# Performance work log

Measured on AMD Instinct MI355X. Metric: run time of the kernel, lower is better.

## Reference

```python
import jax, jax.numpy as jnp
import numpy as np

N = 100000      # nodes
EG = 600000     # global (knn) edges used by GAT layers
E = 600000      # prediction edges scored by edge_mlp
H = 1           # gat_heads
C = 64          # hidden_dim (per-head out channels)
HC = H * C
EDGE_IN = 2 * HC + 2  # 130
EDGE_HID = EDGE_IN * 4  # 520


def gat_layer(x, W, att_src, att_dst, bias, src, dst):
    # PyG GATConv (concat=True, residual=False, no edge_dim, eval mode)
    n = x.shape[0]
    h = (x @ W).reshape(n, H, C)                      # [N,H,C]
    a_s = jnp.sum(h * att_src, axis=-1)               # [N,H]
    a_d = jnp.sum(h * att_dst, axis=-1)               # [N,H]
    alpha = jax.nn.leaky_relu(a_s[src] + a_d[dst], 0.2)  # [Eg,H]
    amax = jax.ops.segment_max(alpha, dst, num_segments=n)
    amax = jnp.where(jnp.isfinite(amax), amax, 0.0)
    e = jnp.exp(alpha - amax[dst])
    denom = jax.ops.segment_sum(e, dst, num_segments=n)
    w = e / (denom[dst] + 1e-16)                      # scatter-softmax over in-edges of dst
    out = jax.ops.segment_sum(h[src] * w[:, :, None], dst, num_segments=n)
    return out.reshape(n, HC) + bias


def setup_inputs() -> dict:
    key = jax.random.key(0)
    ks = jax.random.split(key, 16)
    glorot = lambda k, shape: jax.random.normal(k, shape, jnp.float32) * np.sqrt(2.0 / (shape[0] + shape[-1]))
    inp = {
        "pos": jax.random.normal(ks[0], (N, 3), jnp.float32),
        "edge_index": jax.random.randint(ks[1], (2, E), 0, N, jnp.int32),
        "global_edge_index": jax.random.randint(ks[2], (2, EG), 0, N, jnp.int32),
        "edge_attr": jax.random.uniform(ks[3], (E, 2), jnp.float32),
        # GAT layer 0 (in=3)
        "W0": glorot(ks[4], (3, HC)),
        "att_src0": glorot(ks[5], (1, H, C)),
        "att_dst0": glorot(ks[6], (1, H, C)),
        "b0": jnp.zeros((HC,), jnp.float32),
        # GAT layer 1 (in=HC)
        "W1": glorot(ks[7], (HC, HC)),
        "att_src1": glorot(ks[8], (1, H, C)),
        "att_dst1": glorot(ks[9], (1, H, C)),
        "b1": jnp.zeros((HC,), jnp.float32),
        # edge MLP: Linear(130,520) -> ELU -> Linear(520,1)
        "Wm1": glorot(ks[10], (EDGE_IN, EDGE_HID)),
        "bm1": jnp.zeros((EDGE_HID,), jnp.float32),
        "Wm2": glorot(ks[11], (EDGE_HID, 1)),
        "bm2": jnp.zeros((1,), jnp.float32),
    }
    return inp


def reference(pos, edge_index, global_edge_index, edge_attr,
              W0, att_src0, att_dst0, b0,
              W1, att_src1, att_dst1, b1,
              Wm1, bm1, Wm2, bm2):
    gsrc, gdst = global_edge_index[0], global_edge_index[1]
    x = pos  # dropout p=0 -> identity
    x = jax.nn.elu(gat_layer(x, W0, att_src0, att_dst0, b0, gsrc, gdst))
    x = jax.nn.elu(gat_layer(x, W1, att_src1, att_dst1, b1, gsrc, gdst))
    # per-edge gather-concat-MLP
    esrc, edst = edge_index[0], edge_index[1]
    ef = jnp.concatenate([x[esrc], x[edst], edge_attr], axis=1)  # [E, 130]
    h = jax.nn.elu(ef @ Wm1 + bm1)
    edge_values = (h @ Wm2 + bm2)[:, 0]  # [E]
    return edge_values
```

## Files before the change

kernel.cpp:

```cpp
#include <hip/hip_runtime.h>

#define KN 100000
#define KEG 600000
#define KE 600000
#define NB 98
#define LOG2E 1.4426950408889634f
#define LN2 0.6931471805599453f

#define FB_PREP 391
#define FB_CVEC 33
#define FB_HIST 2344
#define FB_T0 25000

using u16 = unsigned short;
typedef __bf16 bf16x8 __attribute__((ext_vector_type(8)));
typedef float f32x4 __attribute__((ext_vector_type(4)));
typedef float f32x2 __attribute__((ext_vector_type(2)));

__device__ __forceinline__ float b2f(u16 u) { return __uint_as_float(((unsigned)u) << 16); }
__device__ __forceinline__ u16 f2b(float f) {
  unsigned u = __float_as_uint(f);
  u += 0x7FFF + ((u >> 16) & 1);
  return (u16)(u >> 16);
}
__device__ __forceinline__ int imin(int a, int b) { return a < b ? a : b; }
__device__ __forceinline__ float fexp2(float x) {
#if __has_builtin(__builtin_amdgcn_exp2f)
  return __builtin_amdgcn_exp2f(x);
#else
  return __expf(x * LN2);
#endif
}

__device__ __forceinline__ void gload_lds16(const void* g, void* l) {
  __builtin_amdgcn_global_load_lds(
      (const __attribute__((address_space(1))) unsigned int*)g,
      (__attribute__((address_space(3))) unsigned int*)l,
      16, 0, 0);
}

__global__ __launch_bounds__(256) void k_front(
    const float* __restrict__ pos, const float* __restrict__ W0,
    const float* __restrict__ att_s, const float* __restrict__ att_d,
    const float* __restrict__ wm1, const float* __restrict__ bm1,
    const float* __restrict__ wm2, const float* __restrict__ w1,
    const int* __restrict__ gdst,
    u16* __restrict__ wm1t, u16* __restrict__ w1t, float2* __restrict__ wsc2,
    float* __restrict__ w2sum, int* __restrict__ counts,
    u16* __restrict__ h, float* __restrict__ a_s, float* __restrict__ a_d) {
  int bid = blockIdx.x;
  if (bid < FB_PREP) {
    int idx = bid * 256 + threadIdx.x;
    if (idx < 33 * 5 * 512) {
      int j = idx & 7;
      int lane = (idx >> 3) & 63;
      int f = (idx >> 9) % 5;
      int nt = idx / (512 * 5);
      int n = nt * 16 + (lane & 15);
      float v = 0.f;
      if (n < 520) {
        if (f < 4) {
          int k = f * 32 + (lane >> 4) * 8 + j;
          v = wm1[k * 520 + n] * LOG2E;
        } else {
          int kk = (lane >> 4) * 8 + j;
          if (kk == 0) v = wm1[128 * 520 + n] * LOG2E;
          else if (kk == 1) v = wm1[129 * 520 + n] * LOG2E;
          else if (kk == 2) v = bm1[n] * LOG2E;
        }
      }
      wm1t[idx] = f2b(v);
    }
    if (idx < 33 * 64) {
      int lane = idx & 63, nt = idx >> 6;
      int col = nt * 16 + (lane & 15);
      float w2 = (col < 520) ? wm2[col] : 0.f;
      float2 p; p.x = w2; p.y = -LN2 * w2;
      wsc2[idx] = p;
    }
    if (idx < 4 * 2 * 64 * 8) {
      int j = idx & 7;
      int lane = (idx >> 3) & 63;
      int kt = (idx >> 9) & 1;
      int nt = idx >> 10;
      int n = nt * 16 + (lane & 15);
      int k = kt * 32 + (lane >> 4) * 8 + j;
      w1t[idx] = f2b(w1[k * 64 + n]);
    }
  } else if (bid < FB_PREP + FB_CVEC) {
    int lane = threadIdx.x & 63;
    int w = (bid - FB_PREP) * 4 + (threadIdx.x >> 6);
    float x = 0.f;
    if (w <= 129) {
      const float* row = wm1 + (size_t)w * 520;
#pragma unroll
      for (int j = 0; j < 8; ++j) x += row[j * 64 + lane] * wm2[j * 64 + lane];
      if (lane < 8) x += row[512 + lane] * wm2[512 + lane];
    } else if (w == 130) {
#pragma unroll
      for (int j = 0; j < 8; ++j) x += bm1[j * 64 + lane] * wm2[j * 64 + lane];
      if (lane < 8) x += bm1[512 + lane] * wm2[512 + lane];
    } else if (w == 131) {
#pragma unroll
      for (int j = 0; j < 8; ++j) x += wm2[j * 64 + lane];
      if (lane < 8) x += wm2[512 + lane];
    }
    for (int off = 1; off < 64; off <<= 1) x += __shfl_xor(x, off);
    if (w <= 130 && lane < 16) {
      int f = w >> 5, kk = w & 31;
      int qq = kk >> 3, jj = kk & 7;
      u16 chi = f2b(x);
      float v = (lane == 0) ? x : (lane == 1 ? (x - b2f(chi)) : 0.f);
      wm1t[(33 * 5 + f) * 512 + (qq * 16 + lane) * 8 + jj] = f2b(v);
    } else if (w == 131 && lane == 0) {
      w2sum[0] = x;
    }
  } else if (bid < FB_PREP + FB_CVEC + FB_HIST) {
    int e = (bid - (FB_PREP + FB_CVEC)) * 256 + threadIdx.x;
    if (e < KEG) atomicAdd(counts + gdst[e], 1);
  } else {
    int lane = threadIdx.x & 63;
    int n = (bid - (FB_PREP + FB_CVEC + FB_HIST)) * 4 + (threadIdx.x >> 6);
    float p0 = pos[n * 3 + 0], p1 = pos[n * 3 + 1], p2 = pos[n * 3 + 2];
    float hv = p0 * W0[lane] + p1 * W0[64 + lane] + p2 * W0[128 + lane];
    h[n * 64 + lane] = f2b(hv);
    float s = hv * att_s[lane];
    float d = hv * att_d[lane];
    for (int off = 1; off < 64; off <<= 1) { s += __shfl_xor(s, off); d += __shfl_xor(d, off); }
    if (lane == 0) { a_s[n] = s; a_d[n] = d; }
  }
}


__global__ __launch_bounds__(1024) void k_scan_block(
    const int* __restrict__ counts, int* __restrict__ incl, int* __restrict__ bsum) {
  int gid = blockIdx.x * 1024 + threadIdx.x;
  int lane = threadIdx.x & 63, w = threadIdx.x >> 6;
  int x = (gid < KN) ? counts[gid] : 0;
  for (int off = 1; off < 64; off <<= 1) {
    int y = __shfl_up(x, off);
    if (lane >= off) x += y;
  }
  __shared__ int wtot[16];
  if (lane == 63) wtot[w] = x;
  __syncthreads();
  if (w == 0 && lane < 16) {
    int t = wtot[lane];
    for (int off = 1; off < 16; off <<= 1) {
      int y = __shfl_up(t, off);
      if (lane >= off) t += y;
    }
    wtot[lane] = t;
  }
  __syncthreads();
  if (w > 0) x += wtot[w - 1];
  if (gid < KN) incl[gid] = x;
  if (threadIdx.x == 1023) bsum[blockIdx.x] = x;
}

__global__ __launch_bounds__(64) void k_scan_bsum(const int* __restrict__ bsum, int* __restrict__ boff) {
  int lane = threadIdx.x;
  int x0 = (lane < NB) ? bsum[lane] : 0;
  int x1 = (64 + lane < NB) ? bsum[64 + lane] : 0;
  int i0 = x0, i1 = x1;
  for (int off = 1; off < 64; off <<= 1) {
    int y0 = __shfl_up(i0, off), y1 = __shfl_up(i1, off);
    if (lane >= off) { i0 += y0; i1 += y1; }
  }
  int tot0 = __shfl(i0, 63);
  if (lane < NB) boff[lane] = i0 - x0;
  if (64 + lane < NB) boff[64 + lane] = i1 - x1 + tot0;
}

__global__ __launch_bounds__(1024) void k_scan_final(
    const int* __restrict__ incl, const int* __restrict__ counts,
    const int* __restrict__ boff, int* __restrict__ row_start) {
  int gid = blockIdx.x * 1024 + threadIdx.x;
  if (gid < KN) row_start[gid] = incl[gid] - counts[gid] + boff[blockIdx.x];
}

__global__ __launch_bounds__(256) void k_fill(
    const int* __restrict__ gsrc, const int* __restrict__ gdst,
    const int* __restrict__ row_start, int* __restrict__ cursor,
    int* __restrict__ csr_src) {
  int e = blockIdx.x * 256 + threadIdx.x;
  if (e >= KEG) return;
  int d = gdst[e];
  int pos = atomicAdd(cursor + d, 1);
  csr_src[row_start[d] + pos] = gsrc[e];
}


__global__ __launch_bounds__(256) void k_transform1(
    const u16* __restrict__ x, const u16* __restrict__ w1t,
    const float* __restrict__ att_s, const float* __restrict__ att_d,
    u16* __restrict__ h, float* __restrict__ a_s, float* __restrict__ a_d) {
  int lane = threadIdx.x & 63;
  int wave = threadIdx.x >> 6;
  int nodebase = blockIdx.x * 64 + wave * 16;
  int m = lane & 15, q = lane >> 4;

  int node = imin(nodebase + m, KN - 1);
  const bf16x8* px = (const bf16x8*)(x + node * 64);
  bf16x8 A0 = px[q];
  bf16x8 A1 = px[q + 4];

  const bf16x8* bt = (const bf16x8*)w1t;
  float ps[4] = {0.f, 0.f, 0.f, 0.f};
  float pd[4] = {0.f, 0.f, 0.f, 0.f};
#pragma unroll
  for (int nt = 0; nt < 4; ++nt) {
    int col = nt * 16 + m;
    float asv = att_s[col], adv = att_d[col];
    f32x4 acc = {0.f, 0.f, 0.f, 0.f};
    acc = __builtin_amdgcn_mfma_f32_16x16x32_bf16(A0, bt[(nt * 2 + 0) * 64 + lane], acc, 0, 0, 0);
    acc = __builtin_amdgcn_mfma_f32_16x16x32_bf16(A1, bt[(nt * 2 + 1) * 64 + lane], acc, 0, 0, 0);
#pragma unroll
    for (int r = 0; r < 4; ++r) {
      int rown = nodebase + q * 4 + r;
      if (rown < KN) h[rown * 64 + col] = f2b(acc[r]);
      ps[r] += acc[r] * asv;
      pd[r] += acc[r] * adv;
    }
  }
#pragma unroll
  for (int r = 0; r < 4; ++r) {
    float s = ps[r], d = pd[r];
    s += __shfl_xor(s, 1); d += __shfl_xor(d, 1);
    s += __shfl_xor(s, 2); d += __shfl_xor(d, 2);
    s += __shfl_xor(s, 4); d += __shfl_xor(d, 4);
    s += __shfl_xor(s, 8); d += __shfl_xor(d, 8);
    int rown = nodebase + q * 4 + r;
    if (m == 0 && rown < KN) { a_s[rown] = s; a_d[rown] = d; }
  }
}

__global__ __launch_bounds__(256) void k_gat_agg(
    const int* __restrict__ row_start, const int* __restrict__ counts,
    const int* __restrict__ csr_src, const float* __restrict__ a_s,
    const float* __restrict__ a_d, const u16* __restrict__ h,
    const float* __restrict__ bias, u16* __restrict__ xout) {
  int lane = threadIdx.x & 63;
  int n = blockIdx.x * 4 + (threadIdx.x >> 6);
  int start = row_start[n], deg = counts[n];
  float adn = a_d[n];
  float acc = 0.f, den = 0.f;
  int j = 0;
  for (; j + 4 <= deg; j += 4) {
    int s0 = csr_src[start + j];
    int s1 = csr_src[start + j + 1];
    int s2 = csr_src[start + j + 2];
    int s3 = csr_src[start + j + 3];
    float al0 = a_s[s0] + adn; al0 = al0 > 0.f ? al0 : 0.2f * al0;
    float al1 = a_s[s1] + adn; al1 = al1 > 0.f ? al1 : 0.2f * al1;
    float al2 = a_s[s2] + adn; al2 = al2 > 0.f ? al2 : 0.2f * al2;
    float al3 = a_s[s3] + adn; al3 = al3 > 0.f ? al3 : 0.2f * al3;
    float w0 = __expf(al0), w1 = __expf(al1);
    float w2 = __expf(al2), w3 = __expf(al3);
    float h0 = b2f(h[s0 * 64 + lane]);
    float h1 = b2f(h[s1 * 64 + lane]);
    float h2 = b2f(h[s2 * 64 + lane]);
    float h3 = b2f(h[s3 * 64 + lane]);
    den += (w0 + w1) + (w2 + w3);
    acc += w0 * h0 + w1 * h1 + w2 * h2 + w3 * h3;
  }
  for (; j < deg; ++j) {
    int s0 = csr_src[start + j];
    float al = a_s[s0] + adn; al = al > 0.f ? al : 0.2f * al;
    float w0 = __expf(al);
    den += w0;
    acc += w0 * b2f(h[s0 * 64 + lane]);
  }
  float v = acc / (den + 1e-16f) + bias[lane];
  v = v > 0.f ? v : expm1f(v);
  xout[n * 64 + lane] = f2b(v);
}

__global__ __launch_bounds__(256) void k_edge_mlp(
    const int* __restrict__ eidx, const u16* __restrict__ x2bf,
    const float* __restrict__ eattr, const u16* __restrict__ wm1t,
    const float2* __restrict__ wsc2, const float* __restrict__ w2sum,
    const float* __restrict__ bm2, float* __restrict__ out) {
  __shared__ uint4 Bbuf[2][20 * 64];
  int tid = threadIdx.x;
  int lane = tid & 63;
  int wave = tid >> 6;
  int base = blockIdx.x * 256 + wave * 64;
  int m = lane & 15, q = lane >> 4;

  const uint4* gB = (const uint4*)wm1t;
#pragma unroll
  for (int k = 0; k < 5; ++k)
    gload_lds16(gB + tid + k * 256, &Bbuf[0][tid + k * 256]);

  bf16x8 A[4][4];
#pragma unroll
  for (int s = 0; s < 4; ++s) {
    int row = imin(base + s * 16 + m, KE - 1);
    int es = eidx[row], ed = eidx[KE + row];
    const bf16x8* psrc = (const bf16x8*)(x2bf + es * 64);
    const bf16x8* pdst = (const bf16x8*)(x2bf + ed * 64);
    A[s][0] = psrc[q];
    A[s][1] = psrc[q + 4];
    A[s][2] = pdst[q];
    A[s][3] = pdst[q + 4];
  }
  bf16x8 A5[4];
#pragma unroll
  for (int s = 0; s < 4; ++s) {
    bf16x8 a5 = {0, 0, 0, 0, 0, 0, 0, 0};
    if (q == 0) {
      int row = imin(base + s * 16 + m, KE - 1);
      a5[0] = (__bf16)eattr[row * 2 + 0];
      a5[1] = (__bf16)eattr[row * 2 + 1];
      a5[2] = (__bf16)1.0f;
    }
    A5[s] = a5;
  }

  f32x2 osum[4][2];
#pragma unroll
  for (int s = 0; s < 4; ++s) {
    osum[s][0] = (f32x2){0.f, 0.f};
    osum[s][1] = (f32x2){0.f, 0.f};
  }

  __syncthreads();

#pragma unroll 1
  for (int ch = 0; ch < 9; ++ch) {
    int cur = ch & 1, nxt = cur ^ 1;
    if (ch < 8) {
      const uint4* gs = gB + (ch + 1) * 1280;
#pragma unroll
      for (int k = 0; k < 5; ++k)
        gload_lds16(gs + tid + k * 256, &Bbuf[nxt][tid + k * 256]);
    }
    int lim = (ch == 8) ? 1 : 4;
#pragma unroll 1
    for (int li = 0; li < lim; ++li) {
      int nt = ch * 4 + li;
      const bf16x8* lb = (const bf16x8*)(Bbuf[cur] + li * 5 * 64);
      bf16x8 B0 = lb[0 * 64 + lane];
      bf16x8 B1 = lb[1 * 64 + lane];
      bf16x8 B2 = lb[2 * 64 + lane];
      bf16x8 B3 = lb[3 * 64 + lane];
      bf16x8 B4 = lb[4 * 64 + lane];
      float2 w2 = wsc2[nt * 64 + lane];
#pragma unroll
      for (int s = 0; s < 4; ++s) {
        f32x4 acc = {0.f, 0.f, 0.f, 0.f};
        acc = __builtin_amdgcn_mfma_f32_16x16x32_bf16(A[s][0], B0, acc, 0, 0, 0);
        acc = __builtin_amdgcn_mfma_f32_16x16x32_bf16(A[s][1], B1, acc, 0, 0, 0);
        acc = __builtin_amdgcn_mfma_f32_16x16x32_bf16(A[s][2], B2, acc, 0, 0, 0);
        acc = __builtin_amdgcn_mfma_f32_16x16x32_bf16(A[s][3], B3, acc, 0, 0, 0);
        acc = __builtin_amdgcn_mfma_f32_16x16x32_bf16(A5[s],   B4, acc, 0, 0, 0);
        f32x2 t0 = {fminf(acc[0], 0.f), fminf(acc[1], 0.f)};
        f32x2 t1 = {fminf(acc[2], 0.f), fminf(acc[3], 0.f)};
        f32x2 e0 = {fexp2(t0.x), fexp2(t0.y)};
        f32x2 e1 = {fexp2(t1.x), fexp2(t1.y)};
        osum[s][0] += e0 * w2.x + t0 * w2.y;
        osum[s][1] += e1 * w2.x + t1 * w2.y;
      }
    }
    if (ch < 8) __syncthreads();
  }

  const bf16x8* bt = (const bf16x8*)wm1t;
  bf16x8 L0 = bt[(33 * 5 + 0) * 64 + lane];
  bf16x8 L1 = bt[(33 * 5 + 1) * 64 + lane];
  bf16x8 L2 = bt[(33 * 5 + 2) * 64 + lane];
  bf16x8 L3 = bt[(33 * 5 + 3) * 64 + lane];
  bf16x8 L4 = bt[(33 * 5 + 4) * 64 + lane];
  float w2s = w2sum[0];
  float b2v = bm2[0];

#pragma unroll
  for (int s = 0; s < 4; ++s) {
    f32x4 accL = {0.f, 0.f, 0.f, 0.f};
    accL = __builtin_amdgcn_mfma_f32_16x16x32_bf16(A[s][0], L0, accL, 0, 0, 0);
    accL = __builtin_amdgcn_mfma_f32_16x16x32_bf16(A[s][1], L1, accL, 0, 0, 0);
    accL = __builtin_amdgcn_mfma_f32_16x16x32_bf16(A[s][2], L2, accL, 0, 0, 0);
    accL = __builtin_amdgcn_mfma_f32_16x16x32_bf16(A[s][3], L3, accL, 0, 0, 0);
    accL = __builtin_amdgcn_mfma_f32_16x16x32_bf16(A5[s],   L4, accL, 0, 0, 0);
    float ov[4] = {osum[s][0].x, osum[s][0].y, osum[s][1].x, osum[s][1].y};
#pragma unroll
    for (int r = 0; r < 4; ++r) {
      float lin = accL[r] + __shfl_xor(accL[r], 1);
      float v = ov[r];
      v += __shfl_xor(v, 1);
      v += __shfl_xor(v, 2);
      v += __shfl_xor(v, 4);
      v += __shfl_xor(v, 8);
      if (m == 0) {
        int row = base + s * 16 + q * 4 + r;
        if (row < KE) out[row] = v - w2s + lin + b2v;
      }
    }
  }
}

extern "C" void kernel_launch(void* const* d_in, const int* in_sizes, int n_in,
                              void* d_out, int out_size, void* d_ws, size_t ws_size,
                              hipStream_t stream) {
  const float* pos  = (const float*)d_in[0];
  const int* eidx   = (const int*)d_in[1];
  const int* geidx  = (const int*)d_in[2];
  const float* eattr= (const float*)d_in[3];
  const float* W0   = (const float*)d_in[4];
  const float* as0  = (const float*)d_in[5];
  const float* ad0  = (const float*)d_in[6];
  const float* b0   = (const float*)d_in[7];
  const float* W1   = (const float*)d_in[8];
  const float* as1  = (const float*)d_in[9];
  const float* ad1  = (const float*)d_in[10];
  const float* b1   = (const float*)d_in[11];
  const float* Wm1  = (const float*)d_in[12];
  const float* bm1  = (const float*)d_in[13];
  const float* Wm2  = (const float*)d_in[14];
  const float* bm2  = (const float*)d_in[15];
  float* out = (float*)d_out;

  char* ws = (char*)d_ws;
  size_t off = 0;
  auto carve = [&](size_t bytes) {
    char* p = ws + off;
    off = (off + bytes + 255) & ~(size_t)255;
    return p;
  };
  int* counts    = (int*)carve((size_t)KN * 4);
  int* cursor    = (int*)carve((size_t)KN * 4);
  int* incl      = (int*)carve((size_t)KN * 4);
  int* row_start = (int*)carve((size_t)KN * 4);
  int* bsum      = (int*)carve(128 * 4);
  int* boff      = (int*)carve(128 * 4);
  int* csr_src   = (int*)carve((size_t)KEG * 4);
  u16* h         = (u16*)carve((size_t)KN * 64 * 2);
  u16* x12       = (u16*)carve((size_t)KN * 64 * 2);
  float* a_s     = (float*)carve((size_t)KN * 4);
  float* a_d     = (float*)carve((size_t)KN * 4);
  u16* wm1t      = (u16*)carve((size_t)36 * 5 * 512 * 2);
  u16* w1t       = (u16*)carve((size_t)4 * 2 * 64 * 8 * 2);
  float2* wsc2   = (float2*)carve((size_t)33 * 64 * 8);
  float* w2sum   = (float*)carve(256);

  const int* gsrc = geidx;
  const int* gdst = geidx + KEG;

  hipMemsetAsync(d_ws, 0, 800128, stream);

  k_front<<<FB_PREP + FB_CVEC + FB_HIST + FB_T0, 256, 0, stream>>>(
      pos, W0, as0, ad0, Wm1, bm1, Wm2, W1, gdst,
      wm1t, w1t, wsc2, w2sum, counts, h, a_s, a_d);

  k_scan_block<<<NB, 1024, 0, stream>>>(counts, incl, bsum);
  k_scan_bsum<<<1, 64, 0, stream>>>(bsum, boff);
  k_scan_final<<<NB, 1024, 0, stream>>>(incl, counts, boff, row_start);
  k_fill<<<(KEG + 255) / 256, 256, 0, stream>>>(gsrc, gdst, row_start, cursor, csr_src);

  k_gat_agg<<<KN / 4, 256, 0, stream>>>(row_start, counts, csr_src, a_s, a_d, h, b0, x12);

  k_transform1<<<(KN + 63) / 64, 256, 0, stream>>>(x12, w1t, as1, ad1, h, a_s, a_d);
  k_gat_agg<<<KN / 4, 256, 0, stream>>>(row_start, counts, csr_src, a_s, a_d, h, b1, x12);

  k_edge_mlp<<<(KE + 255) / 256, 256, 0, stream>>>(eidx, x12, eattr, wm1t, wsc2, w2sum, bm2, out);
}
```

Measured before the change: 390.8 us.

## Fuse layer-0 GAT aggregation with layer-1 linear transform via shared memory

Merges the first GAT aggregation kernel and the layer-1 MFMA transform into one kernel. Each wave aggregates 16 nodes sequentially, applies ELU, and stores the bf16 features in LDS, which then feed the MFMA transform directly. This removes one launch and the global write and re-read of the intermediate x12 features. In exchange, each wave walks its 16 nodes serially, so there is less parallelism and latency hiding during the gather phase. Separate h and attention buffers are allocated per layer so the fused kernel does not overwrite its own inputs.

```diff
diff --git a/kernel.cpp b/kernel.cpp
--- a/kernel.cpp
+++ b/kernel.cpp
@@ -191,19 +191,62 @@
 }
 
 
-__global__ __launch_bounds__(256) void k_transform1(
-    const u16* __restrict__ x, const u16* __restrict__ w1t,
-    const float* __restrict__ att_s, const float* __restrict__ att_d,
-    u16* __restrict__ h, float* __restrict__ a_s, float* __restrict__ a_d) {
+__global__ __launch_bounds__(256) void k_aggt1(
+    const int* __restrict__ row_start, const int* __restrict__ counts,
+    const int* __restrict__ csr_src, const float* __restrict__ a_s0,
+    const float* __restrict__ a_d0, const u16* __restrict__ h0,
+    const float* __restrict__ b0, const u16* __restrict__ w1t,
+    const float* __restrict__ as1, const float* __restrict__ ad1,
+    u16* __restrict__ h1, float* __restrict__ a_s1, float* __restrict__ a_d1) {
+  __shared__ u16 xb[64][72];
   int lane = threadIdx.x & 63;
   int wave = threadIdx.x >> 6;
-  int nodebase = blockIdx.x * 64 + wave * 16;
+  int nb = blockIdx.x * 64;
+  int nodebase = nb + wave * 16;
+
+  for (int i = 0; i < 16; ++i) {
+    int n = nodebase + i;
+    float v = 0.f;
+    if (n < KN) {
+      int start = row_start[n], deg = counts[n];
+      float adn = a_d0[n];
+      float acc = 0.f, den = 0.f;
+      int j = 0;
+      for (; j + 4 <= deg; j += 4) {
+        int s0 = csr_src[start + j];
+        int s1 = csr_src[start + j + 1];
+        int s2 = csr_src[start + j + 2];
+        int s3 = csr_src[start + j + 3];
+        float al0 = a_s0[s0] + adn; al0 = al0 > 0.f ? al0 : 0.2f * al0;
+        float al1 = a_s0[s1] + adn; al1 = al1 > 0.f ? al1 : 0.2f * al1;
+        float al2 = a_s0[s2] + adn; al2 = al2 > 0.f ? al2 : 0.2f * al2;
+        float al3 = a_s0[s3] + adn; al3 = al3 > 0.f ? al3 : 0.2f * al3;
+        float w0 = __expf(al0), w1 = __expf(al1);
+        float w2 = __expf(al2), w3 = __expf(al3);
+        float h0v = b2f(h0[s0 * 64 + lane]);
+        float h1v = b2f(h0[s1 * 64 + lane]);
+        float h2v = b2f(h0[s2 * 64 + lane]);
+        float h3v = b2f(h0[s3 * 64 + lane]);
+        den += (w0 + w1) + (w2 + w3);
+        acc += w0 * h0v + w1 * h1v + w2 * h2v + w3 * h3v;
+      }
+      for (; j < deg; ++j) {
+        int s0 = csr_src[start + j];
+        float al = a_s0[s0] + adn; al = al > 0.f ? al : 0.2f * al;
+        float w0 = __expf(al);
+        den += w0;
+        acc += w0 * b2f(h0[s0 * 64 + lane]);
+      }
+      v = acc / (den + 1e-16f) + b0[lane];
+      v = v > 0.f ? v : expm1f(v);
+    }
+    xb[wave * 16 + i][lane] = f2b(v);
+  }
+
   int m = lane & 15, q = lane >> 4;
-
-  int node = imin(nodebase + m, KN - 1);
-  const bf16x8* px = (const bf16x8*)(x + node * 64);
-  bf16x8 A0 = px[q];
-  bf16x8 A1 = px[q + 4];
+  const u16* row = xb[wave * 16 + m];
+  bf16x8 A0 = *(const bf16x8*)(row + q * 8);
+  bf16x8 A1 = *(const bf16x8*)(row + 32 + q * 8);
 
   const bf16x8* bt = (const bf16x8*)w1t;
   float ps[4] = {0.f, 0.f, 0.f, 0.f};
@@ -211,14 +254,14 @@
 #pragma unroll
   for (int nt = 0; nt < 4; ++nt) {
     int col = nt * 16 + m;
-    float asv = att_s[col], adv = att_d[col];
+    float asv = as1[col], adv = ad1[col];
     f32x4 acc = {0.f, 0.f, 0.f, 0.f};
     acc = __builtin_amdgcn_mfma_f32_16x16x32_bf16(A0, bt[(nt * 2 + 0) * 64 + lane], acc, 0, 0, 0);
     acc = __builtin_amdgcn_mfma_f32_16x16x32_bf16(A1, bt[(nt * 2 + 1) * 64 + lane], acc, 0, 0, 0);
 #pragma unroll
     for (int r = 0; r < 4; ++r) {
       int rown = nodebase + q * 4 + r;
-      if (rown < KN) h[rown * 64 + col] = f2b(acc[r]);
+      if (rown < KN) h1[rown * 64 + col] = f2b(acc[r]);
       ps[r] += acc[r] * asv;
       pd[r] += acc[r] * adv;
     }
@@ -231,7 +274,7 @@
     s += __shfl_xor(s, 4); d += __shfl_xor(d, 4);
     s += __shfl_xor(s, 8); d += __shfl_xor(d, 8);
     int rown = nodebase + q * 4 + r;
-    if (m == 0 && rown < KN) { a_s[rown] = s; a_d[rown] = d; }
+    if (m == 0 && rown < KN) { a_s1[rown] = s; a_d1[rown] = d; }
   }
 }
 
@@ -435,10 +478,13 @@
   int* bsum      = (int*)carve(128 * 4);
   int* boff      = (int*)carve(128 * 4);
   int* csr_src   = (int*)carve((size_t)KEG * 4);
-  u16* h         = (u16*)carve((size_t)KN * 64 * 2);
+  u16* h0        = (u16*)carve((size_t)KN * 64 * 2);
+  u16* h1        = (u16*)carve((size_t)KN * 64 * 2);
   u16* x12       = (u16*)carve((size_t)KN * 64 * 2);
-  float* a_s     = (float*)carve((size_t)KN * 4);
-  float* a_d     = (float*)carve((size_t)KN * 4);
+  float* a_s0    = (float*)carve((size_t)KN * 4);
+  float* a_d0    = (float*)carve((size_t)KN * 4);
+  float* a_s1    = (float*)carve((size_t)KN * 4);
+  float* a_d1    = (float*)carve((size_t)KN * 4);
   u16* wm1t      = (u16*)carve((size_t)36 * 5 * 512 * 2);
   u16* w1t       = (u16*)carve((size_t)4 * 2 * 64 * 8 * 2);
   float2* wsc2   = (float2*)carve((size_t)33 * 64 * 8);
@@ -451,17 +497,18 @@
 
   k_front<<<FB_PREP + FB_CVEC + FB_HIST + FB_T0, 256, 0, stream>>>(
       pos, W0, as0, ad0, Wm1, bm1, Wm2, W1, gdst,
-      wm1t, w1t, wsc2, w2sum, counts, h, a_s, a_d);
+      wm1t, w1t, wsc2, w2sum, counts, h0, a_s0, a_d0);
 
   k_scan_block<<<NB, 1024, 0, stream>>>(counts, incl, bsum);
   k_scan_bsum<<<1, 64, 0, stream>>>(bsum, boff);
   k_scan_final<<<NB, 1024, 0, stream>>>(incl, counts, boff, row_start);
   k_fill<<<(KEG + 255) / 256, 256, 0, stream>>>(gsrc, gdst, row_start, cursor, csr_src);
 
-  k_gat_agg<<<KN / 4, 256, 0, stream>>>(row_start, counts, csr_src, a_s, a_d, h, b0, x12);
-
-  k_transform1<<<(KN + 63) / 64, 256, 0, stream>>>(x12, w1t, as1, ad1, h, a_s, a_d);
-  k_gat_agg<<<KN / 4, 256, 0, stream>>>(row_start, counts, csr_src, a_s, a_d, h, b1, x12);
+  k_aggt1<<<(KN + 63) / 64, 256, 0, stream>>>(row_start, counts, csr_src,
+                                              a_s0, a_d0, h0, b0,
+                                              w1t, as1, ad1, h1, a_s1, a_d1);
+
+  k_gat_agg<<<KN / 4, 256, 0, stream>>>(row_start, counts, csr_src, a_s1, a_d1, h1, b1, x12);
 
   k_edge_mlp<<<(KE + 255) / 256, 256, 0, stream>>>(eidx, x12, eattr, wm1t, wsc2, w2sum, bm2, out);
 }
```

Result: no change. 386.0 us (-1.2%).
